# Performance work log

Hardware: AMD Instinct MI355X
Metric: run time of the kernel (lower is better)

## Reference

```python
import jax, jax.numpy as jnp
import numpy as np

EPS = 1e-8
MIN_VAL = -1e7  # min_val for masked_max padding


def _cos(v1, v2, axis=-1):
    # torch.F.cosine_similarity: dot / (max(||v1||,eps) * max(||v2||,eps))
    n1 = jnp.maximum(jnp.linalg.norm(v1, axis=axis), EPS)
    n2 = jnp.maximum(jnp.linalg.norm(v2, axis=axis), EPS)
    return jnp.sum(v1 * v2, axis=axis) / (n1 * n2)


def _mpm(v1, v2, w):
    # v1: (B,S,H), v2: (B,S,H) or (B,1,H), w: (P,H)
    mv_one = _cos(v1, v2)[..., None]                 # (B,S,1)
    v1w = w[None, None] * v1[:, :, None, :]          # (B,S,P,H)
    v2w = w[None, None] * v2[:, :, None, :]          # (B,S or 1,P,H)
    mv_many = _cos(v1w, v2w)                          # (B,S,P)
    return mv_one, mv_many


def _mpm_pairwise(v1, v2, w):
    # v1: (B,S1,H), v2: (B,S2,H), w: (P,H) -> (B,S1,S2,P)
    v1w = w[None, :, None, :] * v1[:, None]          # (B,P,S1,H)
    v2w = w[None, :, None, :] * v2[:, None]          # (B,P,S2,H)
    n1 = jnp.linalg.norm(v1w, axis=3)[..., None]     # (B,P,S1,1)
    n2 = jnp.linalg.norm(v2w, axis=3)[..., None]     # (B,P,S2,1)
    mul = jnp.einsum('bpih,bpjh->bpij', v1w, v2w)    # (B,P,S1,S2)
    norm = jnp.maximum(n1 * jnp.swapaxes(n2, 2, 3), EPS)
    return jnp.transpose(mul / norm, (0, 2, 3, 1))


def _masked_max(v, m, axis, keepdims=False):
    return jnp.max(v + (1.0 - m) * MIN_VAL, axis=axis, keepdims=keepdims)


def _masked_mean(v, m, axis, keepdims=False):
    s = jnp.sum(v, axis=axis, keepdims=keepdims)
    c = jnp.sum(m, axis=axis, keepdims=keepdims)
    return s / jnp.maximum(c, EPS)


def _bimpm(context_p, mask_p, context_h, mask_h, w_full, w_maxpool, w_att, w_maxatt):
    mp = mask_p.astype(context_p.dtype)              # (B,S1)
    mh = mask_h.astype(context_h.dtype)              # (B,S2)
    len_p = jnp.sum(mask_p, axis=1)
    len_h = jnp.sum(mask_h, axis=1)
    cp = context_p * mp[..., None]
    ch = context_h * mh[..., None]

    # pairwise cosine similarity (B,S1,S2)
    cos = _cos(cp[:, :, None, :], ch[:, None, :, :])
    cos_max_p = _masked_max(cos, mh[:, None, :], 2, True)
    cos_mean_p = _masked_mean(cos, mh[:, None, :], 2, True)
    cosT = jnp.swapaxes(cos, 1, 2)
    cos_max_h = _masked_max(cosT, mp[:, None, :], 2, True)
    cos_mean_h = _masked_mean(cosT, mp[:, None, :], 2, True)
    mv_p = [cos_max_p, cos_mean_p]
    mv_h = [cos_max_h, cos_mean_h]

    # full match (is_forward=True -> use last valid token)
    B, _, H = cp.shape
    idx_p = jnp.maximum(len_p - 1, 0)[:, None, None]
    idx_h = jnp.maximum(len_h - 1, 0)[:, None, None]
    last_p = jnp.take_along_axis(cp, jnp.broadcast_to(idx_p, (B, 1, H)), axis=1)
    last_h = jnp.take_along_axis(ch, jnp.broadcast_to(idx_h, (B, 1, H)), axis=1)
    o, m = _mpm(cp, last_h, w_full); mv_p += [o, m]
    o, m = _mpm(ch, last_p, w_full); mv_h += [o, m]

    # maxpool match over pairwise multi-perspective cosines (B,S1,S2,P)
    pw = _mpm_pairwise(cp, ch, w_maxpool)
    mv_p += [_masked_max(pw, mh[:, None, :, None], 2),
             _masked_mean(pw, mh[:, None, :, None], 2)]
    pwT = jnp.transpose(pw, (0, 2, 1, 3))
    mv_h += [_masked_max(pwT, mp[:, None, :, None], 2),
             _masked_mean(pwT, mp[:, None, :, None], 2)]

    # attentive match (mean-weighted by cosine attention)
    att = cos
    att_mean_h = jnp.einsum('bij,bjh->bih', att, ch) / jnp.maximum(
        jnp.sum(att, axis=2, keepdims=True), EPS)        # (B,S1,H)
    att_mean_p = jnp.einsum('bij,bih->bjh', att, cp) / jnp.maximum(
        jnp.swapaxes(jnp.sum(att, axis=1, keepdims=True), 1, 2), EPS)  # (B,S2,H)
    o, m = _mpm(cp, att_mean_h, w_att); mv_p += [o, m]
    o, m = _mpm(ch, att_mean_p, w_att); mv_h += [o, m]

    # max attentive match
    att_h_full = ch[:, None, :, :] * att[..., None]      # (B,S1,S2,H)
    att_max_h = _masked_max(att_h_full, mh[:, None, :, None], 2)  # (B,S1,H)
    att_p_full = cp[:, :, None, :] * att[..., None]      # (B,S1,S2,H)
    att_max_p = _masked_max(att_p_full, mp[:, :, None, None], 1)  # (B,S2,H)
    o, m = _mpm(cp, att_max_h, w_maxatt); mv_p += [o, m]
    o, m = _mpm(ch, att_max_p, w_maxatt); mv_h += [o, m]

    # (2, B, S, output_dim=105)
    return jnp.stack([jnp.concatenate(mv_p, axis=-1),
                      jnp.concatenate(mv_h, axis=-1)], axis=0)


def setup_inputs() -> dict:
    B, S1, S2, H, P = 8, 256, 256, 100, 20
    key = jax.random.key(0)
    ks = jax.random.split(key, 8)
    context_p = jax.random.normal(ks[0], (B, S1, H), jnp.float32)
    context_h = jax.random.normal(ks[1], (B, S2, H), jnp.float32)
    len_p = jax.random.randint(ks[2], (B,), S1 // 2, S1 + 1)
    len_h = jax.random.randint(ks[3], (B,), S2 // 2, S2 + 1)
    mask_p = (jnp.arange(S1)[None, :] < len_p[:, None]).astype(jnp.int32)
    mask_h = (jnp.arange(S2)[None, :] < len_h[:, None]).astype(jnp.int32)
    # four matching weights (share_weight_between_directions=True), torch.rand -> U[0,1)
    w_full = jax.random.uniform(ks[4], (P, H), jnp.float32)
    w_maxpool = jax.random.uniform(ks[5], (P, H), jnp.float32)
    w_att = jax.random.uniform(ks[6], (P, H), jnp.float32)
    w_maxatt = jax.random.uniform(ks[7], (P, H), jnp.float32)
    return {"context_p": context_p, "mask_p": mask_p, "context_h": context_h,
            "mask_h": mask_h, "w_full": w_full, "w_maxpool": w_maxpool,
            "w_att": w_att, "w_maxatt": w_maxatt}


def reference(context_p, mask_p, context_h, mask_h, w_full, w_maxpool, w_att, w_maxatt):
    return _bimpm(context_p, mask_p, context_h, mask_h, w_full, w_maxpool, w_att, w_maxatt)
```

## Files before the change

kernel.cpp:

```cpp
#include <hip/hip_runtime.h>

#define Bq 8
#define Sq 256
#define Hq 100
#define Pq 20
#define PPq 21
#define Fq 105
#define EPSq 1e-8f
#define NEGB -1e30f
#define IMG (128 * 136)

typedef short bf16x8 __attribute__((ext_vector_type(8)));
typedef float f32x4 __attribute__((ext_vector_type(4)));

__device__ __forceinline__ unsigned fkey(float f) {
    unsigned b = __float_as_uint(f);
    return (b & 0x80000000u) ? ~b : (b | 0x80000000u);
}
__device__ __forceinline__ float funkey(unsigned k) {
    return __uint_as_float((k & 0x80000000u) ? (k ^ 0x80000000u) : ~k);
}
__device__ __forceinline__ unsigned short bf16rn(float f) {
    unsigned u = __float_as_uint(f);
    unsigned r = u + 0x7FFFu + ((u >> 16) & 1u);
    return (unsigned short)(r >> 16);
}
__device__ __forceinline__ unsigned mulpack(unsigned pair, float w0, float w1) {
    float f0 = __uint_as_float(pair << 16);
    float f1 = __uint_as_float(pair & 0xFFFF0000u);
    f0 *= w0; f1 *= w1;
    return ((unsigned)bf16rn(f0)) | (((unsigned)bf16rn(f1)) << 16);
}

__global__ __launch_bounds__(256) void k_prep(
    const float* __restrict__ ctx_p, const int* __restrict__ mask_p,
    const float* __restrict__ ctx_h, const int* __restrict__ mask_h,
    const float* __restrict__ w_mp,
    float* __restrict__ vm, float* __restrict__ vmT,
    float* __restrict__ mf, float* __restrict__ wn,
    unsigned short* __restrict__ a16,
    float* __restrict__ lens, int* __restrict__ lasts,
    unsigned* __restrict__ statinit) {
    __shared__ float tileT[Hq * 65];
    __shared__ float w2T[Hq * 20];
    __shared__ float redp[PPq * 4 * 64];
    __shared__ float smf[64];
    __shared__ int ired[256];
    int blk = blockIdx.x;
    int side = blk >> 5;
    int b = (blk >> 2) & 7;
    int sq = blk & 3;
    int s0 = sq * 64;
    int t = threadIdx.x;

    for (int idx = blk * 256 + t; idx < 4 * Bq * PPq * Sq; idx += 64 * 256)
        statinit[idx] = 0u;

    const float* ctx = side ? ctx_h : ctx_p;
    const int* mask = side ? mask_h : mask_p;
    ired[t] = mask[b * Sq + t];
    if (t < 64) smf[t] = (float)mask[b * Sq + s0 + t];
    for (int idx = t; idx < Pq * Hq; idx += 256) {
        int p = idx / Hq, h = idx - p * Hq;
        float w = w_mp[idx];
        w2T[h * 20 + p] = w * w;
    }
    __syncthreads();
    if (sq == 0) {
        for (int o = 128; o; o >>= 1) {
            if (t < o) ired[t] += ired[t + o];
            __syncthreads();
        }
        if (t == 0) {
            int l = ired[0];
            lens[side * Bq + b] = (float)l;
            lasts[side * Bq + b] = l > 0 ? l - 1 : 0;
        }
    }

    unsigned short* abase = a16 + (size_t)(side * Bq + b) * 2 * IMG;
    {
        ushort4 z = {0, 0, 0, 0};
        for (int idx = t; idx < 576; idx += 256) {
            int r = idx / 9, c = idx - r * 9;
            int g = s0 + r;
            *(ushort4*)(abase + (g >> 7) * IMG + (g & 127) * 136 + 100 + c * 4) = z;
        }
    }

    const float4* src = (const float4*)(ctx + ((size_t)b * Sq + s0) * Hq);
    float4* vmo = (float4*)(vm + ((size_t)side * Bq + b) * Sq * Hq + (size_t)s0 * Hq);
#pragma unroll
    for (int q = 0; q < 7; q++) {
        int F = t + 256 * q;
        if (F < 1600) {
            int s = F / 25, c = F - s * 25;
            float m = smf[s];
            float4 v4 = src[F];
            v4.x *= m; v4.y *= m; v4.z *= m; v4.w *= m;
            vmo[F] = v4;
            int h0 = c * 4;
            tileT[(h0 + 0) * 65 + s] = v4.x;
            tileT[(h0 + 1) * 65 + s] = v4.y;
            tileT[(h0 + 2) * 65 + s] = v4.z;
            tileT[(h0 + 3) * 65 + s] = v4.w;
            int g = s0 + s;
            ushort4 o;
            o.x = bf16rn(v4.x); o.y = bf16rn(v4.y); o.z = bf16rn(v4.z); o.w = bf16rn(v4.w);
            *(ushort4*)(abase + (g >> 7) * IMG + (g & 127) * 136 + c * 4) = o;
        }
    }
    __syncthreads();

    int sl = t & 63, hq = t >> 6;
    float acc[PPq];
#pragma unroll
    for (int p = 0; p < PPq; p++) acc[p] = 0.f;
    float* vmTo = vmT + ((size_t)side * Bq + b) * Hq * Sq + s0;
    int hbeg = hq * 25;
#pragma unroll 5
    for (int h = hbeg; h < hbeg + 25; h++) {
        float v = tileT[h * 65 + sl];
        vmTo[(size_t)h * Sq + sl] = v;
        float e = v * v;
        acc[Pq] += e;
        const float4* wrow = (const float4*)(w2T + h * 20);
#pragma unroll
        for (int pq = 0; pq < 5; pq++) {
            float4 w4 = wrow[pq];
            acc[pq * 4 + 0] += w4.x * e;
            acc[pq * 4 + 1] += w4.y * e;
            acc[pq * 4 + 2] += w4.z * e;
            acc[pq * 4 + 3] += w4.w * e;
        }
    }
#pragma unroll
    for (int p = 0; p < PPq; p++)
        redp[(p * 4 + hq) * 64 + sl] = acc[p];
    __syncthreads();

    float* wout = wn + ((size_t)side * Bq + b) * PPq * Sq + s0;
    for (int idx = t; idx < PPq * 64; idx += 256) {
        int p = idx >> 6, s2 = idx & 63;
        float ssum = redp[(p * 4 + 0) * 64 + s2] + redp[(p * 4 + 1) * 64 + s2] +
                     redp[(p * 4 + 2) * 64 + s2] + redp[(p * 4 + 3) * 64 + s2];
        wout[p * Sq + s2] = 1.f / fmaxf(sqrtf(ssum), EPSq);
    }
    if (t < 64) mf[(size_t)side * Bq * Sq + b * Sq + s0 + t] = smf[t];
}

__global__ __launch_bounds__(256) void k_pw(
    const unsigned short* __restrict__ a16,
    const float* __restrict__ vmT,
    const float* __restrict__ wn, const float* __restrict__ mf,
    const float* __restrict__ w_mp, const float* __restrict__ lens,
    float* __restrict__ out, float* __restrict__ cosm, float* __restrict__ cosT,
    unsigned* __restrict__ rowmax, float* __restrict__ rowsum,
    unsigned* __restrict__ colmax, float* __restrict__ colsum) {
    __shared__ unsigned short As[IMG];
    __shared__ unsigned short Bs[IMG];
    __shared__ float w2s[144];
    int blk = blockIdx.x;
    int t = threadIdx.x;

    if (blk >= 64) {
        int mblk = blk - 64;
        int b = mblk / 80;
        int rem = mblk - b * 80;
        int p = rem >> 2;
        int ih = (rem >> 1) & 1, jh = rem & 1;
        int i0 = ih * 128, j0 = jh * 128;

        if (t < 144) {
            float w = (t < Hq) ? w_mp[p * Hq + t] : 0.f;
            w2s[t] = w * w;
        }
        __syncthreads();

        {
            const uint4* sa = (const uint4*)(a16 + (size_t)(b * 2 + ih) * IMG);
            uint4* dA = (uint4*)As;
#pragma unroll
            for (int q = 0; q < 9; q++) {
                int idx = t + 256 * q;
                if (idx < 2176) dA[idx] = sa[idx];
            }
        }
        {
            const uint4* sb = (const uint4*)(a16 + (size_t)((Bq + b) * 2 + jh) * IMG);
            uint4* dB = (uint4*)Bs;
#pragma unroll
            for (int q = 0; q < 9; q++) {
                int idx = t + 256 * q;
                if (idx < 2176) {
                    int cc = idx - (idx / 17) * 17;
                    int hb = cc * 8;
                    uint4 ch = sb[idx];
                    float4 wA = *(const float4*)(w2s + hb);
                    float4 wB = *(const float4*)(w2s + hb + 4);
                    uint4 o;
                    o.x = mulpack(ch.x, wA.x, wA.y);
                    o.y = mulpack(ch.y, wA.z, wA.w);
                    o.z = mulpack(ch.z, wB.x, wB.y);
                    o.w = mulpack(ch.w, wB.z, wB.w);
                    dB[idx] = o;
                }
            }
        }
        __syncthreads();

        int lane = t & 63;
        int wv = t >> 6;
        int wr = wv & 1, wc = wv >> 1;
        int lm = lane & 15, lq = lane >> 4;

        f32x4 acc[4][4];
#pragma unroll
        for (int tm = 0; tm < 4; tm++)
#pragma unroll
            for (int tn = 0; tn < 4; tn++) acc[tm][tn] = 0.f;

#pragma unroll
        for (int ks = 0; ks < 4; ks++) {
            bf16x8 af[4], bfr[4];
#pragma unroll
            for (int tm = 0; tm < 4; tm++)
                af[tm] = *(const bf16x8*)&As[(wr * 64 + tm * 16 + lm) * 136 + ks * 32 + lq * 8];
#pragma unroll
            for (int tn = 0; tn < 4; tn++)
                bfr[tn] = *(const bf16x8*)&Bs[(wc * 64 + tn * 16 + lm) * 136 + ks * 32 + lq * 8];
#pragma unroll
            for (int tm = 0; tm < 4; tm++)
#pragma unroll
                for (int tn = 0; tn < 4; tn++)
                    acc[tm][tn] = __builtin_amdgcn_mfma_f32_16x16x32_bf16(af[tm], bfr[tn], acc[tm][tn], 0, 0, 0);
        }

        const float* wn0 = wn + ((size_t)b * PPq + p) * Sq;
        const float* wn1 = wn + ((size_t)(Bq + b) * PPq + p) * Sq;
        const float* mfp = mf + b * Sq;
        const float* mfh = mf + (size_t)Bq * Sq + b * Sq;
        size_t base = ((size_t)b * PPq + p) * Sq;
        float rn2v[4], mzh[4];
#pragma unroll
        for (int tn = 0; tn < 4; tn++) {
            int jj = j0 + wc * 64 + tn * 16 + lm;
            rn2v[tn] = wn1[jj];
            mzh[tn] = mfh[jj] > 0.5f ? 0.f : NEGB;
        }
        float cmax[4] = {NEGB, NEGB, NEGB, NEGB};
        float csum[4] = {0.f, 0.f, 0.f, 0.f};
#pragma unroll
        for (int tm = 0; tm < 4; tm++) {
            int ibase = i0 + wr * 64 + tm * 16 + lq * 4;
            float rn1v[4], mzp[4];
#pragma unroll
            for (int r2 = 0; r2 < 4; r2++) {
                rn1v[r2] = wn0[ibase + r2];
                mzp[r2] = mfp[ibase + r2] > 0.5f ? 0.f : NEGB;
            }
            float rmax[4] = {NEGB, NEGB, NEGB, NEGB};
            float rsum[4] = {0.f, 0.f, 0.f, 0.f};
#pragma unroll
            for (int tn = 0; tn < 4; tn++)
#pragma unroll
                for (int r2 = 0; r2 < 4; r2++) {
                    float v = acc[tm][tn][r2] * rn1v[r2] * rn2v[tn];
                    rmax[r2] = fmaxf(rmax[r2], v + mzh[tn]);
                    rsum[r2] += v;
                    cmax[tn] = fmaxf(cmax[tn], v + mzp[r2]);
                    csum[tn] += v;
                }
#pragma unroll
            for (int r2 = 0; r2 < 4; r2++)
#pragma unroll
                for (int o = 1; o < 16; o <<= 1) {
                    rmax[r2] = fmaxf(rmax[r2], __shfl_xor(rmax[r2], o, 64));
                    rsum[r2] += __shfl_xor(rsum[r2], o, 64);
                }
            if (lm == 0) {
#pragma unroll
                for (int r2 = 0; r2 < 4; r2++) {
                    atomicMax(rowmax + base + ibase + r2, fkey(rmax[r2]));
                    atomicAdd(rowsum + base + ibase + r2, rsum[r2]);
                }
            }
        }
#pragma unroll
        for (int tn = 0; tn < 4; tn++) {
#pragma unroll
            for (int o = 16; o < 64; o <<= 1) {
                cmax[tn] = fmaxf(cmax[tn], __shfl_xor(cmax[tn], o, 64));
                csum[tn] += __shfl_xor(csum[tn], o, 64);
            }
        }
        if (lq == 0) {
#pragma unroll
            for (int tn = 0; tn < 4; tn++) {
                int jj = j0 + wc * 64 + tn * 16 + lm;
                atomicMax(colmax + base + jj, fkey(cmax[tn]));
                atomicAdd(colsum + base + jj, csum[tn]);
            }
        }
        return;
    }

    float (*cbmax)[Sq] = (float (*)[Sq])As;
    float (*cbsum)[Sq] = (float (*)[Sq])(As + 8192);
    int b = blk >> 3, it = blk & 7;
    int lane = t & 63;
    int wid = __builtin_amdgcn_readfirstlane(t >> 6);
    int i0 = it * 32 + wid * 8;

    const float* abase2 = vmT + (size_t)b * Hq * Sq;
    const float* bbase2 = vmT + (size_t)(Bq + b) * Hq * Sq;

    float4 acc[8];
#pragma unroll
    for (int k = 0; k < 8; k++) acc[k] = make_float4(0.f, 0.f, 0.f, 0.f);

#pragma unroll 4
    for (int h = 0; h < Hq; h++) {
        float4 bq = ((const float4*)(bbase2 + h * Sq))[lane];
        const float4* ap = (const float4*)(abase2 + h * Sq + i0);
        float4 a0 = ap[0], a1 = ap[1];
        float av[8] = {a0.x, a0.y, a0.z, a0.w, a1.x, a1.y, a1.z, a1.w};
#pragma unroll
        for (int k = 0; k < 8; k++) {
            acc[k].x += av[k] * bq.x; acc[k].y += av[k] * bq.y;
            acc[k].z += av[k] * bq.z; acc[k].w += av[k] * bq.w;
        }
    }

    const float* wn0 = wn + ((size_t)b * PPq + Pq) * Sq;
    const float* wn1 = wn + ((size_t)(Bq + b) * PPq + Pq) * Sq;
    float4 rn2 = ((const float4*)wn1)[lane];
    float4 mh4 = ((const float4*)(mf + (size_t)Bq * Sq + b * Sq))[lane];
    float invLh = 1.f / fmaxf(lens[Bq + b], EPSq);

    float cmax[4] = {NEGB, NEGB, NEGB, NEGB};
    float csum[4] = {0.f, 0.f, 0.f, 0.f};
#pragma unroll
    for (int k = 0; k < 8; k++) {
        float r1 = wn0[i0 + k];
        float4 v;
        v.x = acc[k].x * r1 * rn2.x;
        v.y = acc[k].y * r1 * rn2.y;
        v.z = acc[k].z * r1 * rn2.z;
        v.w = acc[k].w * r1 * rn2.w;
        float m0 = mh4.x > 0.5f ? v.x : NEGB;
        float m1 = mh4.y > 0.5f ? v.y : NEGB;
        float m2 = mh4.z > 0.5f ? v.z : NEGB;
        float m3 = mh4.w > 0.5f ? v.w : NEGB;
        float rmax = fmaxf(fmaxf(m0, m1), fmaxf(m2, m3));
        float rs = v.x + v.y + v.z + v.w;
        for (int o = 32; o; o >>= 1) {
            rmax = fmaxf(rmax, __shfl_xor(rmax, o, 64));
            rs += __shfl_xor(rs, o, 64);
        }
        if (lane == 0) {
            float* orow = out + ((size_t)(b * Sq + i0 + k)) * Fq;
            orow[0] = rmax;
            orow[1] = rs * invLh;
        }
        float mi = mf[b * Sq + i0 + k];
        if (mi > 0.5f) {
            cmax[0] = fmaxf(cmax[0], v.x); cmax[1] = fmaxf(cmax[1], v.y);
            cmax[2] = fmaxf(cmax[2], v.z); cmax[3] = fmaxf(cmax[3], v.w);
        }
        csum[0] += v.x; csum[1] += v.y; csum[2] += v.z; csum[3] += v.w;
        ((float4*)(cosm + (size_t)(b * Sq + i0 + k) * Sq))[lane] = v;
        int jb = 4 * lane;
        cosT[((size_t)b * Sq + jb + 0) * Sq + i0 + k] = v.x;
        cosT[((size_t)b * Sq + jb + 1) * Sq + i0 + k] = v.y;
        cosT[((size_t)b * Sq + jb + 2) * Sq + i0 + k] = v.z;
        cosT[((size_t)b * Sq + jb + 3) * Sq + i0 + k] = v.w;
    }
    ((float4*)&cbmax[wid][0])[lane] = make_float4(cmax[0], cmax[1], cmax[2], cmax[3]);
    ((float4*)&cbsum[wid][0])[lane] = make_float4(csum[0], csum[1], csum[2], csum[3]);
    __syncthreads();
    {
        int j = t;
        float mx = fmaxf(fmaxf(cbmax[0][j], cbmax[1][j]), fmaxf(cbmax[2][j], cbmax[3][j]));
        float sm = cbsum[0][j] + cbsum[1][j] + cbsum[2][j] + cbsum[3][j];
        size_t cidx = ((size_t)b * PPq + Pq) * Sq + j;
        atomicMax(colmax + cidx, fkey(mx));
        atomicAdd(colsum + cidx, sm);
    }
}

__global__ __launch_bounds__(512) void k_att(
    const float* __restrict__ vm, const float* __restrict__ mf,
    const float* __restrict__ cosm, const float* __restrict__ cosT,
    const unsigned* __restrict__ rowmax, const float* __restrict__ rowsum,
    const unsigned* __restrict__ colmax, const float* __restrict__ colsum,
    const float* __restrict__ lens,
    float* __restrict__ out,
    float* __restrict__ attvT) {
    __shared__ float L[Sq * 8];
    __shared__ float bm[Sq];
    __shared__ float pam[2][4][256];
    __shared__ float pax[2][4][256];
    int blk = blockIdx.x;
    int t = threadIdx.x;

    if (t < 256) {
        if (blk < Bq * PPq) {
            int bcf = blk / PPq, pcf = blk - bcf * PPq;
            float mx = funkey(colmax[(size_t)blk * Sq + t]);
            float sm = colsum[(size_t)blk * Sq + t];
            float invLp = 1.f / fmaxf(lens[bcf], EPSq);
            float* orow = out + (size_t)Bq * Sq * Fq + (size_t)(bcf * Sq + t) * Fq;
            if (pcf < Pq) { orow[23 + pcf] = mx; orow[43 + pcf] = sm * invLp; }
            else { orow[0] = mx; orow[1] = sm * invLp; }
        } else if (blk < 2 * Bq * PPq) {
            int rf = blk - Bq * PPq;
            int bcf = rf / PPq, pcf = rf - bcf * PPq;
            if (pcf < Pq) {
                float mx = funkey(rowmax[(size_t)(bcf * PPq + pcf) * Sq + t]);
                float sm = rowsum[(size_t)(bcf * PPq + pcf) * Sq + t];
                float invLh = 1.f / fmaxf(lens[Bq + bcf], EPSq);
                float* orow = out + (size_t)(bcf * Sq + t) * Fq;
                orow[23 + pcf] = mx; orow[43 + pcf] = sm * invLh;
            }
        }
        bm[t] = (mf[(size_t)(1 - (blk >> 8)) * Bq * Sq + ((blk & 255) >> 5) * Sq + t] > 0.5f) ? 0.f : NEGB;
    }

    int d = blk >> 8;
    int rem = blk & 255;
    int b = rem >> 5, rt = rem & 31;
    int r0 = rt * 8;
    int h = t & 127, rh = (t >> 7) & 1, kh = t >> 8;

    const float* src = (d ? cosm : cosT) + (size_t)b * Sq * Sq;
    {
        int k = t >> 1, c = t & 1;
        float4 v4 = *(const float4*)(src + (size_t)k * Sq + r0 + c * 4);
        *(float4*)(L + k * 8 + c * 4) = v4;
    }
    __syncthreads();

    const float* vB = vm + (size_t)(1 - d) * Bq * Sq * Hq + (size_t)b * Sq * Hq + h;
    bool hv = (h < Hq);
    float am[4] = {0.f, 0.f, 0.f, 0.f};
    float ax[4] = {NEGB, NEGB, NEGB, NEGB};
    int k0 = kh * 128;
#pragma unroll 16
    for (int kk = 0; kk < 128; kk++) {
        int k = k0 + kk;
        float v = hv ? vB[(size_t)k * Hq] : 0.f;
        float4 w = *(const float4*)(L + k * 8 + rh * 4);
        float bk = bm[k];
        float p0 = w.x * v, p1 = w.y * v, p2 = w.z * v, p3 = w.w * v;
        am[0] += p0; am[1] += p1; am[2] += p2; am[3] += p3;
        ax[0] = fmaxf(ax[0], p0 + bk); ax[1] = fmaxf(ax[1], p1 + bk);
        ax[2] = fmaxf(ax[2], p2 + bk); ax[3] = fmaxf(ax[3], p3 + bk);
    }
    int hr = t & 255;
#pragma unroll
    for (int r = 0; r < 4; r++) { pam[kh][r][hr] = am[r]; pax[kh][r][hr] = ax[r]; }
    __syncthreads();
    if (t < 256 && hv) {
        int rb = r0 + rh * 4;
        float4 m4, x4;
        m4.x = pam[0][0][t] + pam[1][0][t]; x4.x = fmaxf(pax[0][0][t], pax[1][0][t]);
        m4.y = pam[0][1][t] + pam[1][1][t]; x4.y = fmaxf(pax[0][1][t], pax[1][1][t]);
        m4.z = pam[0][2][t] + pam[1][2][t]; x4.z = fmaxf(pax[0][2][t], pax[1][2][t]);
        m4.w = pam[0][3][t] + pam[1][3][t]; x4.w = fmaxf(pax[0][3][t], pax[1][3][t]);
        *(float4*)(attvT + (((size_t)(d * 2 + 0) * Bq + b) * Hq + h) * Sq + rb) = m4;
        *(float4*)(attvT + (((size_t)(d * 2 + 1) * Bq + b) * Hq + h) * Sq + rb) = x4;
    }
}

__global__ __launch_bounds__(128) void k_final(
    const float* __restrict__ vm, const float* __restrict__ vmT,
    const int* __restrict__ lasts, const float* __restrict__ attvT,
    const float* __restrict__ w_full, const float* __restrict__ w_att,
    const float* __restrict__ w_maxatt,
    float* __restrict__ out) {
    __shared__ float w2s[Hq * 2];
    __shared__ float v2u[Hq];
    int blk = blockIdx.x;
    int m = blk / 320;
    int rem = blk - m * 320;
    int dir = rem / 160; rem -= dir * 160;
    int b = rem / 20;    rem -= b * 20;
    int sc = rem / 10;
    int ps = rem - sc * 10;
    int t = threadIdx.x;
    const float* W = (m == 0) ? w_full : (m == 1) ? w_att : w_maxatt;
    for (int idx = t; idx < 2 * Hq; idx += 128) {
        int pp = idx / Hq, h = idx - pp * Hq;
        float w = W[(ps * 2 + pp) * Hq + h];
        w2s[h * 2 + pp] = w * w;
    }
    if (m == 0 && t < Hq) {
        int lastO = dir ? lasts[b] : lasts[Bq + b];
        v2u[t] = vm[(size_t)(1 - dir) * Bq * Sq * Hq + ((size_t)b * Sq + lastO) * Hq + t];
    }
    __syncthreads();

    int s = sc * 128 + t;
    const float* v1T = vmT + (size_t)(dir * Bq + b) * Hq * Sq + s;
    const float* v2T = attvT + ((size_t)(dir * 2 + (m == 2 ? 1 : 0)) * Bq + b) * Hq * Sq + s;

    float d0 = 0.f, a0 = 0.f, b0 = 0.f;
    float d1 = 0.f, a1 = 0.f, b1 = 0.f;
    float pd = 0.f, p1 = 0.f, p2 = 0.f;
#pragma unroll 4
    for (int h = 0; h < Hq; h++) {
        float v1 = v1T[h * Sq];
        float v2 = (m == 0) ? v2u[h] : v2T[h * Sq];
        float e1 = v1 * v2, e2 = v1 * v1, e3 = v2 * v2;
        float w0 = w2s[h * 2], w1 = w2s[h * 2 + 1];
        d0 += w0 * e1; a0 += w0 * e2; b0 += w0 * e3;
        d1 += w1 * e1; a1 += w1 * e2; b1 += w1 * e3;
        if (ps == 0) { pd += e1; p1 += e2; p2 += e3; }
    }
    int fbase = (m == 0) ? 2 : (m == 1) ? 63 : 84;
    float* orow = out + (size_t)dir * Bq * Sq * Fq + ((size_t)b * Sq + s) * Fq;
    if (ps == 0)
        orow[fbase] = pd / (fmaxf(sqrtf(p1), EPSq) * fmaxf(sqrtf(p2), EPSq));
    orow[fbase + 1 + ps * 2]     = d0 / (fmaxf(sqrtf(a0), EPSq) * fmaxf(sqrtf(b0), EPSq));
    orow[fbase + 1 + ps * 2 + 1] = d1 / (fmaxf(sqrtf(a1), EPSq) * fmaxf(sqrtf(b1), EPSq));
}

extern "C" void kernel_launch(void* const* d_in, const int* in_sizes, int n_in,
                              void* d_out, int out_size, void* d_ws, size_t ws_size,
                              hipStream_t stream) {
    (void)in_sizes; (void)n_in; (void)out_size; (void)ws_size;
    const float* ctx_p    = (const float*)d_in[0];
    const int*   mask_p   = (const int*)d_in[1];
    const float* ctx_h    = (const float*)d_in[2];
    const int*   mask_h   = (const int*)d_in[3];
    const float* w_full   = (const float*)d_in[4];
    const float* w_maxpool= (const float*)d_in[5];
    const float* w_att    = (const float*)d_in[6];
    const float* w_maxatt = (const float*)d_in[7];
    float* out = (float*)d_out;
    float* ws = (float*)d_ws;

    const size_t BSH = (size_t)Bq * Sq * Hq;
    const size_t BS  = (size_t)Bq * Sq;
    const size_t BSS = (size_t)Bq * Sq * Sq;
    const size_t BPS = (size_t)Bq * PPq * Sq;

    float* vm     = ws;               ws += 2 * BSH;
    float* vmT    = ws;               ws += 2 * BSH;
    unsigned short* a16 = (unsigned short*)ws;  ws += 2 * Bq * IMG / 2 * 2;
    float* mf     = ws;               ws += 2 * BS;
    float* wn     = ws;               ws += 2 * BPS;
    float* cosm   = ws;               ws += BSS;
    float* cosT   = ws;               ws += BSS;
    unsigned* rowmax = (unsigned*)ws; ws += BPS;
    float* rowsum = ws;               ws += BPS;
    unsigned* colmax = (unsigned*)ws; ws += BPS;
    float* colsum = ws;               ws += BPS;
    float* attvT  = ws;               ws += 4 * BSH;
    float* lens   = ws;               ws += 16;
    int*   lasts  = (int*)ws;         ws += 16;

    k_prep<<<64, 256, 0, stream>>>(ctx_p, mask_p, ctx_h, mask_h, w_maxpool,
                                   vm, vmT, mf, wn, a16, lens, lasts, rowmax);
    k_pw<<<704, 256, 0, stream>>>(a16, vmT, wn, mf, w_maxpool, lens,
                                  out, cosm, cosT, rowmax, rowsum, colmax, colsum);
    k_att<<<512, 512, 0, stream>>>(vm, mf, cosm, cosT, rowmax, rowsum, colmax, colsum,
                                   lens, out, attvT);
    k_final<<<960, 128, 0, stream>>>(vm, vmT, lasts, attvT, w_full, w_att, w_maxatt, out);
}
```

Measured before the change: 135.5 us.

## Halve LDS in pairwise MFMA kernel via K-chunking; shrink attention block to 256 threads

The pairwise matching kernel now stages the bf16 A/B tiles in two K-halves of 64 columns instead of the full 128-wide image. This halves the shared-memory footprint so more blocks can be resident per CU, at the cost of an extra sync pair per chunk. The attention kernel drops from 512 to 256 threads, with each thread accumulating 8 rows instead of 4. That raises per-thread register use and ILP but reduces block size and shared scratch.

New measurement: 136.1 us, median of 2. About the same (+0.5%).

```diff
diff --git a/kernel.cpp b/kernel.cpp
--- a/kernel.cpp
+++ b/kernel.cpp
@@ -157,8 +157,8 @@
     float* __restrict__ out, float* __restrict__ cosm, float* __restrict__ cosT,
     unsigned* __restrict__ rowmax, float* __restrict__ rowsum,
     unsigned* __restrict__ colmax, float* __restrict__ colsum) {
-    __shared__ unsigned short As[IMG];
-    __shared__ unsigned short Bs[IMG];
+    __shared__ unsigned short As[128 * 72];
+    __shared__ unsigned short Bs[128 * 72];
     __shared__ float w2s[144];
     int blk = blockIdx.x;
     int t = threadIdx.x;
@@ -177,37 +177,10 @@
         }
         __syncthreads();
 
-        {
-            const uint4* sa = (const uint4*)(a16 + (size_t)(b * 2 + ih) * IMG);
-            uint4* dA = (uint4*)As;
-#pragma unroll
-            for (int q = 0; q < 9; q++) {
-                int idx = t + 256 * q;
-                if (idx < 2176) dA[idx] = sa[idx];
-            }
-        }
-        {
-            const uint4* sb = (const uint4*)(a16 + (size_t)((Bq + b) * 2 + jh) * IMG);
-            uint4* dB = (uint4*)Bs;
-#pragma unroll
-            for (int q = 0; q < 9; q++) {
-                int idx = t + 256 * q;
-                if (idx < 2176) {
-                    int cc = idx - (idx / 17) * 17;
-                    int hb = cc * 8;
-                    uint4 ch = sb[idx];
-                    float4 wA = *(const float4*)(w2s + hb);
-                    float4 wB = *(const float4*)(w2s + hb + 4);
-                    uint4 o;
-                    o.x = mulpack(ch.x, wA.x, wA.y);
-                    o.y = mulpack(ch.y, wA.z, wA.w);
-                    o.z = mulpack(ch.z, wB.x, wB.y);
-                    o.w = mulpack(ch.w, wB.z, wB.w);
-                    dB[idx] = o;
-                }
-            }
-        }
-        __syncthreads();
+        const uint4* sa = (const uint4*)(a16 + (size_t)(b * 2 + ih) * IMG);
+        const uint4* sb = (const uint4*)(a16 + (size_t)((Bq + b) * 2 + jh) * IMG);
+        uint4* dA = (uint4*)As;
+        uint4* dB = (uint4*)Bs;
 
         int lane = t & 63;
         int wv = t >> 6;
@@ -221,19 +194,40 @@
             for (int tn = 0; tn < 4; tn++) acc[tm][tn] = 0.f;
 
 #pragma unroll
-        for (int ks = 0; ks < 4; ks++) {
-            bf16x8 af[4], bfr[4];
-#pragma unroll
-            for (int tm = 0; tm < 4; tm++)
-                af[tm] = *(const bf16x8*)&As[(wr * 64 + tm * 16 + lm) * 136 + ks * 32 + lq * 8];
-#pragma unroll
-            for (int tn = 0; tn < 4; tn++)
-                bfr[tn] = *(const bf16x8*)&Bs[(wc * 64 + tn * 16 + lm) * 136 + ks * 32 + lq * 8];
-#pragma unroll
-            for (int tm = 0; tm < 4; tm++)
+        for (int q = 0; q < 2; q++) {
+#pragma unroll
+            for (int it = 0; it < 4; it++) {
+                int idx = t + 256 * it;
+                int row = idx >> 3, cc = idx & 7;
+                dA[row * 9 + cc] = sa[row * 17 + q * 8 + cc];
+                int hb = (q * 8 + cc) * 8;
+                uint4 ch = sb[row * 17 + q * 8 + cc];
+                float4 wA = *(const float4*)(w2s + hb);
+                float4 wB = *(const float4*)(w2s + hb + 4);
+                uint4 o;
+                o.x = mulpack(ch.x, wA.x, wA.y);
+                o.y = mulpack(ch.y, wA.z, wA.w);
+                o.z = mulpack(ch.z, wB.x, wB.y);
+                o.w = mulpack(ch.w, wB.z, wB.w);
+                dB[row * 9 + cc] = o;
+            }
+            __syncthreads();
+#pragma unroll
+            for (int ksl = 0; ksl < 2; ksl++) {
+                bf16x8 af[4], bfr[4];
+#pragma unroll
+                for (int tm = 0; tm < 4; tm++)
+                    af[tm] = *(const bf16x8*)&As[(wr * 64 + tm * 16 + lm) * 72 + ksl * 32 + lq * 8];
 #pragma unroll
                 for (int tn = 0; tn < 4; tn++)
-                    acc[tm][tn] = __builtin_amdgcn_mfma_f32_16x16x32_bf16(af[tm], bfr[tn], acc[tm][tn], 0, 0, 0);
+                    bfr[tn] = *(const bf16x8*)&Bs[(wc * 64 + tn * 16 + lm) * 72 + ksl * 32 + lq * 8];
+#pragma unroll
+                for (int tm = 0; tm < 4; tm++)
+#pragma unroll
+                    for (int tn = 0; tn < 4; tn++)
+                        acc[tm][tn] = __builtin_amdgcn_mfma_f32_16x16x32_bf16(af[tm], bfr[tn], acc[tm][tn], 0, 0, 0);
+            }
+            __syncthreads();
         }
 
         const float* wn0 = wn + ((size_t)b * PPq + p) * Sq;
@@ -306,7 +300,7 @@
     }
 
     float (*cbmax)[Sq] = (float (*)[Sq])As;
-    float (*cbsum)[Sq] = (float (*)[Sq])(As + 8192);
+    float (*cbsum)[Sq] = (float (*)[Sq])(As + 4096);
     int b = blk >> 3, it = blk & 7;
     int lane = t & 63;
     int wid = __builtin_amdgcn_readfirstlane(t >> 6);
@@ -389,7 +383,7 @@
     }
 }
 
-__global__ __launch_bounds__(512) void k_att(
+__global__ __launch_bounds__(256) void k_att(
     const float* __restrict__ vm, const float* __restrict__ mf,
     const float* __restrict__ cosm, const float* __restrict__ cosT,
     const unsigned* __restrict__ rowmax, const float* __restrict__ rowsum,
@@ -399,77 +393,85 @@
     float* __restrict__ attvT) {
     __shared__ float L[Sq * 8];
     __shared__ float bm[Sq];
-    __shared__ float pam[2][4][256];
-    __shared__ float pax[2][4][256];
+    __shared__ float pam[2][8][128];
+    __shared__ float pax[2][8][128];
     int blk = blockIdx.x;
     int t = threadIdx.x;
-
-    if (t < 256) {
-        if (blk < Bq * PPq) {
-            int bcf = blk / PPq, pcf = blk - bcf * PPq;
-            float mx = funkey(colmax[(size_t)blk * Sq + t]);
-            float sm = colsum[(size_t)blk * Sq + t];
-            float invLp = 1.f / fmaxf(lens[bcf], EPSq);
-            float* orow = out + (size_t)Bq * Sq * Fq + (size_t)(bcf * Sq + t) * Fq;
-            if (pcf < Pq) { orow[23 + pcf] = mx; orow[43 + pcf] = sm * invLp; }
-            else { orow[0] = mx; orow[1] = sm * invLp; }
-        } else if (blk < 2 * Bq * PPq) {
-            int rf = blk - Bq * PPq;
-            int bcf = rf / PPq, pcf = rf - bcf * PPq;
-            if (pcf < Pq) {
-                float mx = funkey(rowmax[(size_t)(bcf * PPq + pcf) * Sq + t]);
-                float sm = rowsum[(size_t)(bcf * PPq + pcf) * Sq + t];
-                float invLh = 1.f / fmaxf(lens[Bq + bcf], EPSq);
-                float* orow = out + (size_t)(bcf * Sq + t) * Fq;
-                orow[23 + pcf] = mx; orow[43 + pcf] = sm * invLh;
-            }
-        }
-        bm[t] = (mf[(size_t)(1 - (blk >> 8)) * Bq * Sq + ((blk & 255) >> 5) * Sq + t] > 0.5f) ? 0.f : NEGB;
-    }
-
     int d = blk >> 8;
     int rem = blk & 255;
     int b = rem >> 5, rt = rem & 31;
     int r0 = rt * 8;
-    int h = t & 127, rh = (t >> 7) & 1, kh = t >> 8;
+
+    if (blk < Bq * PPq) {
+        int bcf = blk / PPq, pcf = blk - bcf * PPq;
+        float mx = funkey(colmax[(size_t)blk * Sq + t]);
+        float sm = colsum[(size_t)blk * Sq + t];
+        float invLp = 1.f / fmaxf(lens[bcf], EPSq);
+        float* orow = out + (size_t)Bq * Sq * Fq + (size_t)(bcf * Sq + t) * Fq;
+        if (pcf < Pq) { orow[23 + pcf] = mx; orow[43 + pcf] = sm * invLp; }
+        else { orow[0] = mx; orow[1] = sm * invLp; }
+    } else if (blk < 2 * Bq * PPq) {
+        int rf = blk - Bq * PPq;
+        int bcf = rf / PPq, pcf = rf - bcf * PPq;
+        if (pcf < Pq) {
+            float mx = funkey(rowmax[(size_t)(bcf * PPq + pcf) * Sq + t]);
+            float sm = rowsum[(size_t)(bcf * PPq + pcf) * Sq + t];
+            float invLh = 1.f / fmaxf(lens[Bq + bcf], EPSq);
+            float* orow = out + (size_t)(bcf * Sq + t) * Fq;
+            orow[23 + pcf] = mx; orow[43 + pcf] = sm * invLh;
+        }
+    }
+    bm[t] = (mf[(size_t)(1 - d) * Bq * Sq + b * Sq + t] > 0.5f) ? 0.f : NEGB;
 
     const float* src = (d ? cosm : cosT) + (size_t)b * Sq * Sq;
-    {
-        int k = t >> 1, c = t & 1;
+#pragma unroll
+    for (int q = 0; q < 2; q++) {
+        int F = t + 256 * q;
+        int k = F >> 1, c = F & 1;
         float4 v4 = *(const float4*)(src + (size_t)k * Sq + r0 + c * 4);
         *(float4*)(L + k * 8 + c * 4) = v4;
     }
     __syncthreads();
 
+    int h = t & 127, kh = t >> 7;
     const float* vB = vm + (size_t)(1 - d) * Bq * Sq * Hq + (size_t)b * Sq * Hq + h;
     bool hv = (h < Hq);
-    float am[4] = {0.f, 0.f, 0.f, 0.f};
-    float ax[4] = {NEGB, NEGB, NEGB, NEGB};
+    float am[8], ax[8];
+#pragma unroll
+    for (int r = 0; r < 8; r++) { am[r] = 0.f; ax[r] = NEGB; }
     int k0 = kh * 128;
 #pragma unroll 16
     for (int kk = 0; kk < 128; kk++) {
         int k = k0 + kk;
         float v = hv ? vB[(size_t)k * Hq] : 0.f;
-        float4 w = *(const float4*)(L + k * 8 + rh * 4);
+        float4 w0 = *(const float4*)(L + k * 8);
+        float4 w1 = *(const float4*)(L + k * 8 + 4);
         float bk = bm[k];
-        float p0 = w.x * v, p1 = w.y * v, p2 = w.z * v, p3 = w.w * v;
-        am[0] += p0; am[1] += p1; am[2] += p2; am[3] += p3;
-        ax[0] = fmaxf(ax[0], p0 + bk); ax[1] = fmaxf(ax[1], p1 + bk);
-        ax[2] = fmaxf(ax[2], p2 + bk); ax[3] = fmaxf(ax[3], p3 + bk);
-    }
-    int hr = t & 255;
-#pragma unroll
-    for (int r = 0; r < 4; r++) { pam[kh][r][hr] = am[r]; pax[kh][r][hr] = ax[r]; }
-    __syncthreads();
-    if (t < 256 && hv) {
-        int rb = r0 + rh * 4;
-        float4 m4, x4;
-        m4.x = pam[0][0][t] + pam[1][0][t]; x4.x = fmaxf(pax[0][0][t], pax[1][0][t]);
-        m4.y = pam[0][1][t] + pam[1][1][t]; x4.y = fmaxf(pax[0][1][t], pax[1][1][t]);
-        m4.z = pam[0][2][t] + pam[1][2][t]; x4.z = fmaxf(pax[0][2][t], pax[1][2][t]);
-        m4.w = pam[0][3][t] + pam[1][3][t]; x4.w = fmaxf(pax[0][3][t], pax[1][3][t]);
-        *(float4*)(attvT + (((size_t)(d * 2 + 0) * Bq + b) * Hq + h) * Sq + rb) = m4;
-        *(float4*)(attvT + (((size_t)(d * 2 + 1) * Bq + b) * Hq + h) * Sq + rb) = x4;
+        float wv[8] = {w0.x, w0.y, w0.z, w0.w, w1.x, w1.y, w1.z, w1.w};
+#pragma unroll
+        for (int r = 0; r < 8; r++) {
+            float pr = wv[r] * v;
+            am[r] += pr;
+            ax[r] = fmaxf(ax[r], pr + bk);
+        }
+    }
+#pragma unroll
+    for (int r = 0; r < 8; r++) { pam[kh][r][h] = am[r]; pax[kh][r][h] = ax[r]; }
+    __syncthreads();
+    if (t < Hq) {
+        float4 m0, m1, x0, x1;
+        m0.x = pam[0][0][t] + pam[1][0][t]; x0.x = fmaxf(pax[0][0][t], pax[1][0][t]);
+        m0.y = pam[0][1][t] + pam[1][1][t]; x0.y = fmaxf(pax[0][1][t], pax[1][1][t]);
+        m0.z = pam[0][2][t] + pam[1][2][t]; x0.z = fmaxf(pax[0][2][t], pax[1][2][t]);
+        m0.w = pam[0][3][t] + pam[1][3][t]; x0.w = fmaxf(pax[0][3][t], pax[1][3][t]);
+        m1.x = pam[0][4][t] + pam[1][4][t]; x1.x = fmaxf(pax[0][4][t], pax[1][4][t]);
+        m1.y = pam[0][5][t] + pam[1][5][t]; x1.y = fmaxf(pax[0][5][t], pax[1][5][t]);
+        m1.z = pam[0][6][t] + pam[1][6][t]; x1.z = fmaxf(pax[0][6][t], pax[1][6][t]);
+        m1.w = pam[0][7][t] + pam[1][7][t]; x1.w = fmaxf(pax[0][7][t], pax[1][7][t]);
+        float* om = attvT + (((size_t)(d * 2 + 0) * Bq + b) * Hq + t) * Sq + r0;
+        float* ox = attvT + (((size_t)(d * 2 + 1) * Bq + b) * Hq + t) * Sq + r0;
+        *(float4*)om = m0; *(float4*)(om + 4) = m1;
+        *(float4*)ox = x0; *(float4*)(ox + 4) = x1;
     }
 }
 
@@ -565,7 +567,7 @@
                                    vm, vmT, mf, wn, a16, lens, lasts, rowmax);
     k_pw<<<704, 256, 0, stream>>>(a16, vmT, wn, mf, w_maxpool, lens,
                                   out, cosm, cosT, rowmax, rowsum, colmax, colsum);
-    k_att<<<512, 512, 0, stream>>>(vm, mf, cosm, cosT, rowmax, rowsum, colmax, colsum,
+    k_att<<<512, 256, 0, stream>>>(vm, mf, cosm, cosT, rowmax, rowsum, colmax, colsum,
                                    lens, out, attvT);
     k_final<<<960, 128, 0, stream>>>(vm, vmT, lasts, attvT, w_full, w_att, w_maxatt, out);
 }
```
